# Optimization experiments

Hardware: AMD Instinct MI355X
Metric: run time of the kernel (lower is better)

## Reference

```python
import math
import jax, jax.numpy as jnp
import numpy as np

PH, PW = 16, 16
MAPPER_X = [0, 0, 6, 0, 0, 1, 1, 4, 5, 1, 3, 0, 0, 0, 3, 2]
MAPPER_Y = [0, 1, 0, 5, 2, 0, 2, 0, 0, 6, 0, 4, 6, 3, 5, 2]


def _make_dct_bases(ph, pw, mapper_x, mapper_y):
    bases = []
    for u, v in zip(mapper_x, mapper_y):
        Bu = np.cos(np.pi * (np.arange(ph) + 0.5) * u / ph) / math.sqrt(ph)
        if u != 0:
            Bu = Bu * math.sqrt(2)
        Bv = np.cos(np.pi * (np.arange(pw) + 0.5) * v / pw) / math.sqrt(pw)
        if v != 0:
            Bv = Bv * math.sqrt(2)
        bases.append(np.outer(Bu, Bv))
    return jnp.asarray(np.stack(bases, axis=0), dtype=jnp.float32)  # [M, ph, pw]


def setup_inputs() -> dict:
    key = jax.random.key(0)
    x = jax.random.normal(key, (16, 64, 224, 224), dtype=jnp.float32)
    dct_bases = _make_dct_bases(PH, PW, MAPPER_X, MAPPER_Y)
    return {"x": x, "dct_bases": dct_bases}


def reference(x, dct_bases):
    # x: [B, C, H, W]; dct_bases: [M, ph, pw]
    B, C, H, W = x.shape
    M, ph, pw = dct_bases.shape
    # H, W chosen divisible by ph, pw -> pad_h = pad_w = 0 (faithful to the no-pad path)
    Hp, Wp = H // ph, W // pw
    x_mean = x.mean(axis=1)                              # [B, H, W]
    patches = x_mean.reshape(B, Hp, ph, Wp, pw)          # non-overlapping unfold
    coeff = jnp.einsum('bhiwj,mij->bmhw', patches, dct_bases)  # [B, M, Hp, Wp]
    # nearest upsample by (ph, pw): broadcast each coeff over its patch footprint
    freq = jnp.broadcast_to(coeff[:, :, :, None, :, None], (B, M, Hp, ph, Wp, pw))
    return freq.reshape(B, M, H, W)
```

## Files before the change

### kernel.cpp

```cpp
#include <hip/hip_runtime.h>

#define B_   16
#define C_   64
#define H_   224
#define W_   224
#define M_   16
#define PH   16
#define PW   16
#define HP   14
#define WP   14
#define PLANE (H_ * W_)
#define PLANE4 (PLANE / 4)
#define BAND  (PH * W_)
#define BAND4 (BAND / 4)
#define LSTRIDE 228

typedef float f4 __attribute__((ext_vector_type(4)));

__global__ __launch_bounds__(256)
void k1_mean(const float* __restrict__ x, float* __restrict__ mean) {
    const int f4i = blockIdx.x * 256 + threadIdx.x;
    const int b   = blockIdx.y;
    const f4* p = (const f4*)x + (size_t)b * C_ * PLANE4 + f4i;
    f4 acc = {0.f, 0.f, 0.f, 0.f};
#pragma unroll 16
    for (int c = 0; c < C_; ++c) {
        f4 v = __builtin_nontemporal_load(&p[(size_t)c * PLANE4]);
        acc += v;
    }
    const float inv = 1.f / (float)C_;
    acc *= inv;
    ((f4*)mean)[(size_t)b * PLANE4 + f4i] = acc;
}

__global__ __launch_bounds__(256)
void k2_dct_write(const float* __restrict__ mean, const float* __restrict__ bases,
                  float* __restrict__ out) {
    const int m  = blockIdx.x;
    const int hp = blockIdx.y;
    const int b  = blockIdx.z;
    const int t  = threadIdx.x;

    __shared__ float band[PH * LSTRIDE];
    __shared__ float cf[WP];

    const f4* src = (const f4*)(mean + (size_t)b * PLANE + (size_t)hp * BAND);
    for (int j = t; j < BAND4; j += 256) {
        const int row  = j / (W_ / 4);
        const int col4 = j % (W_ / 4);
        *(f4*)&band[row * LSTRIDE + col4 * 4] = src[j];
    }
    __syncthreads();

    if (t < WP * 16) {
        const int wp = t >> 4;
        const int s  = t & 15;
        const float* brow = bases + m * (PH * PW) + s * PW;
        float partial = 0.f;
#pragma unroll
        for (int k = 0; k < 16; ++k)
            partial += band[s * LSTRIDE + wp * PW + k] * brow[k];
        partial += __shfl_xor(partial, 1);
        partial += __shfl_xor(partial, 2);
        partial += __shfl_xor(partial, 4);
        partial += __shfl_xor(partial, 8);
        if (s == 0) cf[wp] = partial;
    }
    __syncthreads();

    f4* dst = (f4*)(out + ((size_t)b * M_ + m) * PLANE + (size_t)hp * BAND);
#pragma unroll
    for (int j4 = 0; j4 < BAND4; j4 += 256) {
        const int j    = j4 + t;
        const int col4 = j % (W_ / 4);
        if (j < BAND4) {
            const float c = cf[col4 >> 2];
            f4 v = {c, c, c, c};
            __builtin_nontemporal_store(v, &dst[j]);
        }
    }
}

extern "C" void kernel_launch(void* const* d_in, const int* in_sizes, int n_in,
                              void* d_out, int out_size, void* d_ws, size_t ws_size,
                              hipStream_t stream) {
    const float* x     = (const float*)d_in[0];
    const float* bases = (const float*)d_in[1];
    float* out         = (float*)d_out;

    float* mean = (float*)d_ws;

    dim3 g1(PLANE4 / 256, B_);
    k1_mean<<<g1, 256, 0, stream>>>(x, mean);

    dim3 g2(M_, HP, B_);
    k2_dct_write<<<g2, 256, 0, stream>>>(mean, bases, out);
}
```

Measured before the change: 283.4 us.

## Fuse channel mean, DCT projection and upsample write into one kernel

Combines the two kernels into one. Each block owns a 16-row band and half the width for one batch: it reduces over channels straight into shared memory, computes all 16 DCT coefficients from bases cached in shared memory, and writes all 16 output planes for its tile. This removes the intermediate mean buffer round-trip and one kernel launch, and loads each band once instead of once per frequency. The cost is a much smaller grid (448 blocks), which may leave bandwidth unused during the 64-channel read and the large write phase.

```diff
diff --git a/kernel.cpp b/kernel.cpp
--- a/kernel.cpp
+++ b/kernel.cpp
@@ -9,75 +9,95 @@
 #define PW   16
 #define HP   14
 #define WP   14
-#define PLANE (H_ * W_)
+#define PLANE  (H_ * W_)
 #define PLANE4 (PLANE / 4)
-#define BAND  (PH * W_)
-#define BAND4 (BAND / 4)
-#define LSTRIDE 228
+#define W4     (W_ / 4)
+#define NSPLIT 2
+#define CW     (W_ / NSPLIT)
+#define CW4    (CW / 4)
+#define WPB    (WP / NSPLIT)
+#define SLOTS  (PH * CW4)
+#define LSTW   116
 
 typedef float f4 __attribute__((ext_vector_type(4)));
 
 __global__ __launch_bounds__(256)
-void k1_mean(const float* __restrict__ x, float* __restrict__ mean) {
-    const int f4i = blockIdx.x * 256 + threadIdx.x;
-    const int b   = blockIdx.y;
-    const f4* p = (const f4*)x + (size_t)b * C_ * PLANE4 + f4i;
-    f4 acc = {0.f, 0.f, 0.f, 0.f};
-#pragma unroll 16
-    for (int c = 0; c < C_; ++c) {
-        f4 v = __builtin_nontemporal_load(&p[(size_t)c * PLANE4]);
-        acc += v;
-    }
-    const float inv = 1.f / (float)C_;
-    acc *= inv;
-    ((f4*)mean)[(size_t)b * PLANE4 + f4i] = acc;
-}
-
-__global__ __launch_bounds__(256)
-void k2_dct_write(const float* __restrict__ mean, const float* __restrict__ bases,
-                  float* __restrict__ out) {
-    const int m  = blockIdx.x;
+void k_fused(const float* __restrict__ x, const float* __restrict__ bases,
+             float* __restrict__ out) {
+    const int cb = blockIdx.x;
     const int hp = blockIdx.y;
     const int b  = blockIdx.z;
     const int t  = threadIdx.x;
 
-    __shared__ float band[PH * LSTRIDE];
-    __shared__ float cf[WP];
+    __shared__ float band[PH][LSTW];
+    __shared__ float bs[M_ * PH * PW];
+    __shared__ float cf[M_][WPB];
 
-    const f4* src = (const f4*)(mean + (size_t)b * PLANE + (size_t)hp * BAND);
-    for (int j = t; j < BAND4; j += 256) {
-        const int row  = j / (W_ / 4);
-        const int col4 = j % (W_ / 4);
-        *(f4*)&band[row * LSTRIDE + col4 * 4] = src[j];
+    {
+        const f4* bsrc = (const f4*)bases;
+        f4* bdst = (f4*)bs;
+#pragma unroll
+        for (int i = 0; i < 4; ++i)
+            bdst[t + i * 256] = bsrc[t + i * 256];
+    }
+
+    {
+        const int j0 = t;
+        const int j1 = t + 256;
+        const int r0 = j0 / CW4, c0 = j0 % CW4;
+        const int r1 = j1 / CW4, c1 = j1 % CW4;
+        const f4* p0 = (const f4*)x + (size_t)b * C_ * PLANE4
+                     + (hp * PH + r0) * W4 + cb * CW4 + c0;
+        const f4* p1 = (const f4*)x + (size_t)b * C_ * PLANE4
+                     + (hp * PH + r1) * W4 + cb * CW4 + c1;
+        f4 a0 = {0.f, 0.f, 0.f, 0.f};
+        f4 a1 = {0.f, 0.f, 0.f, 0.f};
+        if (j1 < SLOTS) {
+#pragma unroll 8
+            for (int c = 0; c < C_; ++c) {
+                a0 += __builtin_nontemporal_load(&p0[(size_t)c * PLANE4]);
+                a1 += __builtin_nontemporal_load(&p1[(size_t)c * PLANE4]);
+            }
+        } else {
+#pragma unroll 8
+            for (int c = 0; c < C_; ++c)
+                a0 += __builtin_nontemporal_load(&p0[(size_t)c * PLANE4]);
+        }
+        const float inv = 1.f / (float)C_;
+        a0 *= inv; a1 *= inv;
+        *(f4*)&band[r0][c0 * 4] = a0;
+        if (j1 < SLOTS) *(f4*)&band[r1][c1 * 4] = a1;
     }
     __syncthreads();
 
-    if (t < WP * 16) {
-        const int wp = t >> 4;
-        const int s  = t & 15;
-        const float* brow = bases + m * (PH * PW) + s * PW;
-        float partial = 0.f;
+    if (t < M_ * WPB) {
+        const int m  = t / WPB;
+        const int wp = t % WPB;
+        const float* bm = &bs[m * PH * PW];
+        f4 sv = {0.f, 0.f, 0.f, 0.f};
 #pragma unroll
-        for (int k = 0; k < 16; ++k)
-            partial += band[s * LSTRIDE + wp * PW + k] * brow[k];
-        partial += __shfl_xor(partial, 1);
-        partial += __shfl_xor(partial, 2);
-        partial += __shfl_xor(partial, 4);
-        partial += __shfl_xor(partial, 8);
-        if (s == 0) cf[wp] = partial;
+        for (int r = 0; r < PH; ++r) {
+#pragma unroll
+            for (int q = 0; q < 4; ++q) {
+                f4 bv = *(const f4*)&band[r][wp * PW + q * 4];
+                f4 mv = *(const f4*)&bm[r * PW + q * 4];
+                sv += bv * mv;
+            }
+        }
+        cf[m][wp] = sv.x + sv.y + sv.z + sv.w;
     }
     __syncthreads();
 
-    f4* dst = (f4*)(out + ((size_t)b * M_ + m) * PLANE + (size_t)hp * BAND);
+    f4* dst = (f4*)out + (size_t)(b * M_) * PLANE4 + (hp * PH) * W4 + cb * CW4;
 #pragma unroll
-    for (int j4 = 0; j4 < BAND4; j4 += 256) {
-        const int j    = j4 + t;
-        const int col4 = j % (W_ / 4);
-        if (j < BAND4) {
-            const float c = cf[col4 >> 2];
-            f4 v = {c, c, c, c};
-            __builtin_nontemporal_store(v, &dst[j]);
-        }
+    for (int it = 0; it < (M_ * SLOTS) / 256; ++it) {
+        const int idx = it * 256 + t;
+        const int m   = idx / SLOTS;
+        const int j   = idx % SLOTS;
+        const int r   = j / CW4, c4 = j % CW4;
+        const float v = cf[m][c4 >> 2];
+        f4 vv = {v, v, v, v};
+        __builtin_nontemporal_store(vv, &dst[(size_t)m * PLANE4 + r * W4 + c4]);
     }
 }
 
@@ -88,11 +108,6 @@
     const float* bases = (const float*)d_in[1];
     float* out         = (float*)d_out;
 
-    float* mean = (float*)d_ws;
-
-    dim3 g1(PLANE4 / 256, B_);
-    k1_mean<<<g1, 256, 0, stream>>>(x, mean);
-
-    dim3 g2(M_, HP, B_);
-    k2_dct_write<<<g2, 256, 0, stream>>>(mean, bases, out);
+    dim3 g(NSPLIT, HP, B_);
+    k_fused<<<g, 256, 0, stream>>>(x, bases, out);
 }
```

Result: no change. 282.6 us (-0.3%).
